# Performance work log

Measured on AMD Instinct MI355X. Metric: run time of the kernel, lower is better.

Reference implementation:

```python
import jax, jax.numpy as jnp
import numpy as np

N_OBJ, C_DET, C_SEG, H, W = 1024, 8, 4, 28, 28


def setup_inputs() -> dict:
    key = jax.random.key(0)
    k1, k2, k3 = jax.random.split(key, 3)
    # probabilities exactly as produced upstream in forward():
    # det class probs = logits.softmax(1); det masks = sigmoid probs;
    # seg masks = softmax over seg_class axis (axis=2)
    det_class_probs = jax.nn.softmax(jax.random.normal(k1, (N_OBJ, C_DET)), axis=1)
    det_mask_probs = jax.nn.sigmoid(jax.random.normal(k2, (N_OBJ, C_DET, H, W)))
    seg_mask_probs = jax.nn.softmax(jax.random.normal(k3, (N_OBJ, C_DET, C_SEG, H, W)), axis=2)
    # bipartite graph edges (seg_class i, det_class j), distinct pairs
    edges = np.array([(i, j) for j in range(C_DET) for i in range(C_SEG) if (i + j) % 2 == 0],
                     dtype=np.int64)
    edge_i = jnp.asarray(edges[:, 0])
    edge_j = jnp.asarray(edges[:, 1])
    return {
        'det_class_probs': det_class_probs,
        'det_mask_probs': det_mask_probs,
        'seg_mask_probs': seg_mask_probs,
        'edge_i': edge_i,
        'edge_j': edge_j,
    }


def reference(det_class_probs, det_mask_probs, seg_mask_probs, edge_i, edge_j):
    # Per edge (i, j):
    #   area   = sum_{n,h,w} seg[:, j, i] * det[:, j]
    #   p_area = area / sum_{n,h,w} det[:, j]
    #   p_i_j  = p_area * det_class_probs[:, j]          (shape (N_obj,))
    # probs = sum over edges of p_i_j.
    # Batch all edges: overlap matrix A[j, i] and denominator per det class.
    A = jnp.einsum('ncshw,nchw->cs', seg_mask_probs, det_mask_probs)  # (C_det, C_seg)
    denom = det_mask_probs.sum(axis=(0, 2, 3))                        # (C_det,)
    p_area = A / denom[:, None]                                       # (C_det, C_seg)
    # accumulate per-edge scalar weights onto their det class j
    w = jnp.zeros((A.shape[0],), A.dtype).at[edge_j].add(p_area[edge_j, edge_i])
    probs = det_class_probs @ w                                       # (N_obj,)
    # F.binary_cross_entropy(probs, ones) = mean(-log(probs)), log clamped at -100
    bce_loss = (-jnp.clip(jnp.log(probs), -100.0, None)).mean()
    return bce_loss
```

## Files before the change

kernel.cpp:

```cpp
#include <hip/hip_runtime.h>
#include <math.h>

#define N_OBJ 1024
#define C_DET 8
#define C_SEG 4
#define HW    784
#define HW4   196
#define NBLK  128

typedef float f32x4 __attribute__((ext_vector_type(4)));


__global__ __launch_bounds__(256) void overlap_kernel(
    const float* __restrict__ det,
    const float* __restrict__ seg,
    float* __restrict__ partial)
{
    const int c  = blockIdx.y;
    const int bx = blockIdx.x;
    float accD = 0.f, accA0 = 0.f, accA1 = 0.f, accA2 = 0.f, accA3 = 0.f;

    const int total4 = N_OBJ * HW4;
    const int step   = NBLK * 256;

    auto body = [&](int t4) {
        const int n  = t4 / HW4;
        const int p4 = t4 - n * HW4;
        const int drow = (n * C_DET + c) * HW + p4 * 4;
        const f32x4 d = __builtin_nontemporal_load(
            reinterpret_cast<const f32x4*>(det + drow));
        const int srow = (n * C_DET + c) * (C_SEG * HW) + p4 * 4;
        const f32x4 s0 = __builtin_nontemporal_load(
            reinterpret_cast<const f32x4*>(seg + srow + 0 * HW));
        const f32x4 s1 = __builtin_nontemporal_load(
            reinterpret_cast<const f32x4*>(seg + srow + 1 * HW));
        const f32x4 s2 = __builtin_nontemporal_load(
            reinterpret_cast<const f32x4*>(seg + srow + 2 * HW));
        const f32x4 s3 = __builtin_nontemporal_load(
            reinterpret_cast<const f32x4*>(seg + srow + 3 * HW));
        accD  += (d.x + d.y) + (d.z + d.w);
        accA0 += s0.x * d.x + s0.y * d.y + s0.z * d.z + s0.w * d.w;
        accA1 += s1.x * d.x + s1.y * d.y + s1.z * d.z + s1.w * d.w;
        accA2 += s2.x * d.x + s2.y * d.y + s2.z * d.z + s2.w * d.w;
        accA3 += s3.x * d.x + s3.y * d.y + s3.z * d.z + s3.w * d.w;
    };

    int t4 = bx * 256 + threadIdx.x;
    for (; t4 + step < total4; t4 += 2 * step) {
        body(t4);
        body(t4 + step);
    }
    if (t4 < total4) body(t4);

    __shared__ float sred[5][4];
    const int lane = threadIdx.x & 63;
    const int wv   = threadIdx.x >> 6;
    float vals[5] = {accD, accA0, accA1, accA2, accA3};
    #pragma unroll
    for (int k = 0; k < 5; ++k) {
        float v = vals[k];
        #pragma unroll
        for (int off = 32; off > 0; off >>= 1) v += __shfl_down(v, off, 64);
        if (lane == 0) sred[k][wv] = v;
    }
    __syncthreads();
    if (threadIdx.x < 5) {
        const float v = sred[threadIdx.x][0] + sred[threadIdx.x][1]
                      + sred[threadIdx.x][2] + sred[threadIdx.x][3];
        partial[(c * NBLK + bx) * 5 + threadIdx.x] = v;
    }
}

__global__ __launch_bounds__(256) void finalize_kernel(
    const float* __restrict__ det_class,
    const int* __restrict__ edge_i,
    const int* __restrict__ edge_j,
    const int n_edges,
    const float* __restrict__ partial,
    float* __restrict__ out)
{
    __shared__ float A[C_DET][C_SEG];
    __shared__ float D[C_DET];
    __shared__ float wsh[C_DET];
    const int tid = threadIdx.x;

    if (tid < 40) {
        const int c = tid / 5;
        const int k = tid - c * 5;
        float s = 0.f;
        for (int b = 0; b < NBLK; ++b)
            s += partial[(c * NBLK + b) * 5 + k];
        if (k == 0) D[c] = s;
        else        A[c][k - 1] = s;
    }
    if (tid < C_DET) wsh[tid] = 0.f;
    __syncthreads();

    if (tid < n_edges) {
        const int i = edge_i[tid];
        const int j = edge_j[tid];
        atomicAdd(&wsh[j], A[j][i] / D[j]);
    }
    __syncthreads();

    float wl[C_DET];
    #pragma unroll
    for (int k = 0; k < C_DET; ++k) wl[k] = wsh[k];

    float acc = 0.f;
    for (int n = tid; n < N_OBJ; n += 256) {
        const f32x4 a = *reinterpret_cast<const f32x4*>(det_class + n * C_DET);
        const f32x4 b = *reinterpret_cast<const f32x4*>(det_class + n * C_DET + 4);
        float p = a.x * wl[0] + a.y * wl[1] + a.z * wl[2] + a.w * wl[3]
                + b.x * wl[4] + b.y * wl[5] + b.z * wl[6] + b.w * wl[7];
        acc += -fmaxf(logf(p), -100.f);
    }

    __shared__ float sred[4];
    const int lane = tid & 63;
    const int wv   = tid >> 6;
    float v = acc;
    #pragma unroll
    for (int off = 32; off > 0; off >>= 1) v += __shfl_down(v, off, 64);
    if (lane == 0) sred[wv] = v;
    __syncthreads();
    if (tid == 0) {
        out[0] = (sred[0] + sred[1] + sred[2] + sred[3]) * (1.0f / N_OBJ);
    }
}

extern "C" void kernel_launch(void* const* d_in, const int* in_sizes, int n_in,
                              void* d_out, int out_size, void* d_ws, size_t ws_size,
                              hipStream_t stream) {
    const float* det_class = (const float*)d_in[0];
    const float* det       = (const float*)d_in[1];
    const float* seg       = (const float*)d_in[2];
    const int*   edge_i    = (const int*)d_in[3];
    const int*   edge_j    = (const int*)d_in[4];
    const int    n_edges   = in_sizes[3];
    float* out = (float*)d_out;
    float* partial = (float*)d_ws;

    overlap_kernel<<<dim3(NBLK, C_DET), 256, 0, stream>>>(det, seg, partial);
    finalize_kernel<<<1, 256, 0, stream>>>(det_class, edge_i, edge_j, n_edges,
                                           partial, out);
}
```

Measured before the change: 175.5 us.

## Fuse finalize into overlap kernel via last-block atomic counter

Merges the two kernels into one: each block writes its partial sums, increments a global counter, and the last block to finish does the final reduction, edge weighting and BCE loss. The grid shrinks to 98 blocks per class so every thread runs exactly 8 iterations with no tail check. This removes a second kernel launch and its serialization, but adds a memset launch to reset the counter and a threadfence/atomic on every block.

```diff
diff --git a/kernel.cpp b/kernel.cpp
--- a/kernel.cpp
+++ b/kernel.cpp
@@ -6,22 +6,32 @@
 #define C_SEG 4
 #define HW    784
 #define HW4   196
-#define NBLK  128
+#define NBLK  98
+#define TOTB  (C_DET * NBLK)
+#define NPART (TOTB * 5)
 
 typedef float f32x4 __attribute__((ext_vector_type(4)));
 
 
-__global__ __launch_bounds__(256) void overlap_kernel(
+__global__ __launch_bounds__(256) void fused_kernel(
     const float* __restrict__ det,
     const float* __restrict__ seg,
-    float* __restrict__ partial)
+    const float* __restrict__ det_class,
+    const int* __restrict__ edge_i,
+    const int* __restrict__ edge_j,
+    const int n_edges,
+    float* __restrict__ partial,
+    unsigned* __restrict__ counter,
+    float* __restrict__ out)
 {
-    const int c  = blockIdx.y;
-    const int bx = blockIdx.x;
-    float accD = 0.f, accA0 = 0.f, accA1 = 0.f, accA2 = 0.f, accA3 = 0.f;
+    const int c   = blockIdx.y;
+    const int bx  = blockIdx.x;
+    const int tid = threadIdx.x;
 
-    const int total4 = N_OBJ * HW4;
-    const int step   = NBLK * 256;
+    float accD = 0.f, a0 = 0.f, a1 = 0.f, a2 = 0.f, a3 = 0.f;
+
+    const int base = bx * 256 + tid;
+    const int step = NBLK * 256;
 
     auto body = [&](int t4) {
         const int n  = t4 / HW4;
@@ -38,24 +48,20 @@
             reinterpret_cast<const f32x4*>(seg + srow + 2 * HW));
         const f32x4 s3 = __builtin_nontemporal_load(
             reinterpret_cast<const f32x4*>(seg + srow + 3 * HW));
-        accD  += (d.x + d.y) + (d.z + d.w);
-        accA0 += s0.x * d.x + s0.y * d.y + s0.z * d.z + s0.w * d.w;
-        accA1 += s1.x * d.x + s1.y * d.y + s1.z * d.z + s1.w * d.w;
-        accA2 += s2.x * d.x + s2.y * d.y + s2.z * d.z + s2.w * d.w;
-        accA3 += s3.x * d.x + s3.y * d.y + s3.z * d.z + s3.w * d.w;
+        accD += (d.x + d.y) + (d.z + d.w);
+        a0 += s0.x * d.x + s0.y * d.y + s0.z * d.z + s0.w * d.w;
+        a1 += s1.x * d.x + s1.y * d.y + s1.z * d.z + s1.w * d.w;
+        a2 += s2.x * d.x + s2.y * d.y + s2.z * d.z + s2.w * d.w;
+        a3 += s3.x * d.x + s3.y * d.y + s3.z * d.z + s3.w * d.w;
     };
 
-    int t4 = bx * 256 + threadIdx.x;
-    for (; t4 + step < total4; t4 += 2 * step) {
-        body(t4);
-        body(t4 + step);
-    }
-    if (t4 < total4) body(t4);
+    #pragma unroll 2
+    for (int it = 0; it < 8; ++it) body(base + it * step);
 
     __shared__ float sred[5][4];
-    const int lane = threadIdx.x & 63;
-    const int wv   = threadIdx.x >> 6;
-    float vals[5] = {accD, accA0, accA1, accA2, accA3};
+    const int lane = tid & 63;
+    const int wv   = tid >> 6;
+    float vals[5] = {accD, a0, a1, a2, a3};
     #pragma unroll
     for (int k = 0; k < 5; ++k) {
         float v = vals[k];
@@ -64,42 +70,46 @@
         if (lane == 0) sred[k][wv] = v;
     }
     __syncthreads();
-    if (threadIdx.x < 5) {
-        const float v = sred[threadIdx.x][0] + sred[threadIdx.x][1]
-                      + sred[threadIdx.x][2] + sred[threadIdx.x][3];
-        partial[(c * NBLK + bx) * 5 + threadIdx.x] = v;
+    if (tid < 5) {
+        partial[(c * NBLK + bx) * 5 + tid] =
+            sred[tid][0] + sred[tid][1] + sred[tid][2] + sred[tid][3];
     }
-}
 
-__global__ __launch_bounds__(256) void finalize_kernel(
-    const float* __restrict__ det_class,
-    const int* __restrict__ edge_i,
-    const int* __restrict__ edge_j,
-    const int n_edges,
-    const float* __restrict__ partial,
-    float* __restrict__ out)
-{
-    __shared__ float A[C_DET][C_SEG];
-    __shared__ float D[C_DET];
+    __threadfence();
+    __syncthreads();
+    __shared__ unsigned oldc;
+    if (tid == 0) oldc = atomicAdd(counter, 1u);
+    __syncthreads();
+    if (oldc != TOTB - 1) return;
+
+    f32x4 ra[4], rb[4];
+    #pragma unroll
+    for (int r = 0; r < 4; ++r) {
+        const int n = tid + 256 * r;
+        ra[r] = *reinterpret_cast<const f32x4*>(det_class + n * C_DET);
+        rb[r] = *reinterpret_cast<const f32x4*>(det_class + n * C_DET + 4);
+    }
+
+    __threadfence();
+
+    __shared__ float DA[C_DET * 5];
+    if (tid < C_DET * 5) DA[tid] = 0.f;
+    __syncthreads();
+    for (int f = tid; f < NPART; f += 256) {
+        const int cb = f / 5;
+        const int k  = f - cb * 5;
+        const int cc = cb / NBLK;
+        atomicAdd(&DA[cc * 5 + k], partial[f]);
+    }
+    __syncthreads();
+
     __shared__ float wsh[C_DET];
-    const int tid = threadIdx.x;
-
-    if (tid < 40) {
-        const int c = tid / 5;
-        const int k = tid - c * 5;
-        float s = 0.f;
-        for (int b = 0; b < NBLK; ++b)
-            s += partial[(c * NBLK + b) * 5 + k];
-        if (k == 0) D[c] = s;
-        else        A[c][k - 1] = s;
-    }
     if (tid < C_DET) wsh[tid] = 0.f;
     __syncthreads();
-
     if (tid < n_edges) {
         const int i = edge_i[tid];
         const int j = edge_j[tid];
-        atomicAdd(&wsh[j], A[j][i] / D[j]);
+        atomicAdd(&wsh[j], DA[j * 5 + 1 + i] / DA[j * 5]);
     }
     __syncthreads();
 
@@ -108,25 +118,23 @@
     for (int k = 0; k < C_DET; ++k) wl[k] = wsh[k];
 
     float acc = 0.f;
-    for (int n = tid; n < N_OBJ; n += 256) {
-        const f32x4 a = *reinterpret_cast<const f32x4*>(det_class + n * C_DET);
-        const f32x4 b = *reinterpret_cast<const f32x4*>(det_class + n * C_DET + 4);
-        float p = a.x * wl[0] + a.y * wl[1] + a.z * wl[2] + a.w * wl[3]
-                + b.x * wl[4] + b.y * wl[5] + b.z * wl[6] + b.w * wl[7];
+    #pragma unroll
+    for (int r = 0; r < 4; ++r) {
+        const float p = ra[r].x * wl[0] + ra[r].y * wl[1]
+                      + ra[r].z * wl[2] + ra[r].w * wl[3]
+                      + rb[r].x * wl[4] + rb[r].y * wl[5]
+                      + rb[r].z * wl[6] + rb[r].w * wl[7];
         acc += -fmaxf(logf(p), -100.f);
     }
 
-    __shared__ float sred[4];
-    const int lane = tid & 63;
-    const int wv   = tid >> 6;
+    __shared__ float fred[4];
     float v = acc;
     #pragma unroll
     for (int off = 32; off > 0; off >>= 1) v += __shfl_down(v, off, 64);
-    if (lane == 0) sred[wv] = v;
+    if (lane == 0) fred[wv] = v;
     __syncthreads();
-    if (tid == 0) {
-        out[0] = (sred[0] + sred[1] + sred[2] + sred[3]) * (1.0f / N_OBJ);
-    }
+    if (tid == 0)
+        out[0] = (fred[0] + fred[1] + fred[2] + fred[3]) * (1.0f / N_OBJ);
 }
 
 extern "C" void kernel_launch(void* const* d_in, const int* in_sizes, int n_in,
@@ -140,8 +148,9 @@
     const int    n_edges   = in_sizes[3];
     float* out = (float*)d_out;
     float* partial = (float*)d_ws;
+    unsigned* counter = (unsigned*)((char*)d_ws + NPART * sizeof(float));
 
-    overlap_kernel<<<dim3(NBLK, C_DET), 256, 0, stream>>>(det, seg, partial);
-    finalize_kernel<<<1, 256, 0, stream>>>(det_class, edge_i, edge_j, n_edges,
-                                           partial, out);
+    hipMemsetAsync(counter, 0, sizeof(unsigned), stream);
+    fused_kernel<<<dim3(NBLK, C_DET), 256, 0, stream>>>(
+        det, seg, det_class, edge_i, edge_j, n_edges, partial, counter, out);
 }
```

Result: slower. 301.4 us (+71.8%).
